# Kernel optimization log

Measured on AMD Instinct MI355X. Metric: run time of the kernel, lower is better.

## Reference

```python
import jax, jax.numpy as jnp
import numpy as np

B, S, EH2, DH, A = 128, 1024, 1024, 512, 512

def setup_inputs() -> dict:
    key = jax.random.key(0)
    k1, k2, k3, k4, k5 = jax.random.split(key, 5)
    scale_in = 1.0 / np.sqrt(EH2 + DH)
    scale_a = 1.0 / np.sqrt(A)
    return {
        "encoder_outputs": jax.random.normal(k1, (B, S, EH2), dtype=jnp.float32),
        "decoder_hidden": jax.random.normal(k2, (B, DH), dtype=jnp.float32),
        "src_mask": jnp.ones((B, S), dtype=jnp.int32),
        "W_attn": jax.random.normal(k3, (EH2 + DH, A), dtype=jnp.float32) * scale_in,
        "b_attn": jax.random.normal(k4, (A,), dtype=jnp.float32) * scale_in,
        "v": jax.random.normal(k5, (A,), dtype=jnp.float32) * scale_a,
    }

def reference(encoder_outputs, decoder_hidden, src_mask, W_attn, b_attn, v):
    # Split W_attn into encoder-part and decoder-part to avoid materializing
    # the [B,S,EH2+DH] concat (same math as Linear(cat(enc, dec_repeated))).
    W_enc = W_attn[:EH2]          # [EH2, A]
    W_dec = W_attn[EH2:]          # [DH, A]
    enc_proj = jnp.einsum('bse,ea->bsa', encoder_outputs, W_enc)  # [B,S,A]
    dec_proj = decoder_hidden @ W_dec                              # [B,A]
    energy = jnp.tanh(enc_proj + dec_proj[:, None, :] + b_attn)    # [B,S,A]
    scores = jnp.einsum('bsa,a->bs', energy, v)                    # [B,S]
    scores = jnp.where(src_mask == 0, jnp.float32(-1e10), scores)
    attn_weights = jax.nn.softmax(scores, axis=1)                  # [B,S]
    context = jnp.einsum('bs,bse->be', attn_weights, encoder_outputs)  # [B,EH2]
    return (context, attn_weights)
```

## Files before the change

kernel.cpp:

```cpp
#include <hip/hip_runtime.h>
#include <math.h>

#define BB   128
#define SS   1024
#define EH2  1024
#define DHD  512
#define AD   512
#define MTOT (BB*SS)
#define KDIM 1024

#define BM2   64
#define BK2   32
#define NSTEP (KDIM/BK2)

typedef __attribute__((ext_vector_type(8)))  short short8;
typedef __attribute__((ext_vector_type(16))) float f32x16;

static __device__ __forceinline__ unsigned short f2bf_rne(float x) {
    unsigned u = __float_as_uint(x);
    u += 0x7FFF + ((u >> 16) & 1);
    return (unsigned short)(u >> 16);
}

__global__ __launch_bounds__(256) void k0_wprep(
    const float* __restrict__ W, unsigned short* __restrict__ Wt)
{
    const int g     = blockIdx.x * 256 + threadIdx.x;
    const int lane  = g & 63;
    const int ct    = (g >> 6) & 15;
    const int kk2   = (g >> 10) & 1;
    const int ks    = g >> 11;
    const int col   = ct * 32 + (lane & 31);
    const int kbase = ks * 32 + kk2 * 16 + (lane >> 5) * 8;
    short8 out;
    #pragma unroll
    for (int j = 0; j < 8; ++j)
        out[j] = (short)f2bf_rne(W[(size_t)(kbase + j) * AD + col]);
    *(short8*)&Wt[(size_t)g * 8] = out;
}

__global__ __launch_bounds__(256) void k1_decproj(
    const float* __restrict__ dec,
    const float* __restrict__ Wdec,
    const float* __restrict__ bias,
    float* __restrict__ dec_proj)
{
    __shared__ float dls[DHD];
    const int b = blockIdx.x;
    const int t = threadIdx.x;
    for (int i = t; i < DHD; i += 256) dls[i] = dec[b * DHD + i];
    __syncthreads();
    float acc0 = bias[t];
    float acc1 = bias[t + 256];
    #pragma unroll 8
    for (int k = 0; k < DHD; ++k) {
        const float d = dls[k];
        acc0 += d * Wdec[(size_t)k * AD + t];
        acc1 += d * Wdec[(size_t)k * AD + t + 256];
    }
    dec_proj[b * AD + t]       = acc0;
    dec_proj[b * AD + t + 256] = acc1;
}

#define AS_IDX(hl, kk2, mt) (((hl) * 2 + (kk2)) * 2 + (mt))

__global__ __launch_bounds__(256, 2) void k2_gemm_score(
    const float* __restrict__ enc,
    const unsigned short* __restrict__ Wt,
    const float* __restrict__ dp,
    const float* __restrict__ v,
    float* __restrict__ scores)
{
    __shared__ unsigned short As[2][8][512];
    __shared__ float dp_l[AD], v_l[AD];
    __shared__ float sred[4][BM2];

    const int t     = threadIdx.x;
    const int wn    = t >> 6;
    const int lane  = t & 63;
    const int mbase = blockIdx.x * BM2;
    const int b     = blockIdx.x >> 4;

    dp_l[t]       = dp[b * AD + t];
    dp_l[t + 256] = dp[b * AD + t + 256];
    v_l[t]        = v[t];
    v_l[t + 256]  = v[t + 256];

    const int smt  = (t >> 6) & 1;
    const int skk2 = t >> 7;
    const int srow = smt * 32 + (lane & 31);
    const int skb  = skk2 * 16 + (lane >> 5) * 8;
    const float* aptr = enc + (size_t)(mbase + srow) * KDIM + skb;
    unsigned short* asH = &As[0][AS_IDX(0, skk2, smt)][lane * 8];
    unsigned short* asL = &As[0][AS_IDX(1, skk2, smt)][lane * 8];
    const int asStride = 8 * 512;

    const short8* bbase = (const short8*)Wt + wn * 256 + lane;

#define CONV_WRITE_A(buf_, xa_, xb_) do {                                   \
    const float xs_[8] = {xa_.x, xa_.y, xa_.z, xa_.w, xb_.x, xb_.y, xb_.z, xb_.w}; \
    short8 hi_, lo_;                                                        \
    _Pragma("unroll")                                                       \
    for (int j_ = 0; j_ < 8; ++j_) {                                        \
        const unsigned u_ = __float_as_uint(xs_[j_]);                       \
        hi_[j_] = (short)(u_ >> 16);                                        \
        lo_[j_] = (short)f2bf_rne(xs_[j_] - __uint_as_float(u_ & 0xFFFF0000u)); \
    }                                                                       \
    *(short8*)(asH + (buf_) * asStride) = hi_;                              \
    *(short8*)(asL + (buf_) * asStride) = lo_;                              \
} while (0)

    f32x16 acc[2][4];
    #pragma unroll
    for (int mi = 0; mi < 2; ++mi)
        #pragma unroll
        for (int n = 0; n < 4; ++n) acc[mi][n] = (f32x16)0.f;

    {
        const float4 xa = *(const float4*)(aptr);
        const float4 xb = *(const float4*)(aptr + 4);
        CONV_WRITE_A(0, xa, xb);
    }
    __syncthreads();

#define KSTEP(BUF, ks_)                                                      \
  {                                                                          \
    const bool pf = ((ks_) + 1 < NSTEP);                                     \
    float4 xa, xb;                                                           \
    if (pf) {                                                                \
        xa = *(const float4*)(aptr + ((ks_) + 1) * BK2);                     \
        xb = *(const float4*)(aptr + ((ks_) + 1) * BK2 + 4);                 \
    }                                                                        \
                                                                \
    {                                                                        \
        short8 bfr[4];                                                       \
        _Pragma("unroll")                                                    \
        for (int n = 0; n < 4; ++n) bfr[n] = bbase[(ks_) * 2048 + n * 64];   \
        const short8 aH0 = *(const short8*)&As[BUF][AS_IDX(0,0,0)][lane*8];  \
        const short8 aL0 = *(const short8*)&As[BUF][AS_IDX(1,0,0)][lane*8];  \
        const short8 aH1 = *(const short8*)&As[BUF][AS_IDX(0,0,1)][lane*8];  \
        const short8 aL1 = *(const short8*)&As[BUF][AS_IDX(1,0,1)][lane*8];  \
        __builtin_amdgcn_s_setprio(1);                                       \
        _Pragma("unroll")                                                    \
        for (int n = 0; n < 4; ++n) {                                        \
            acc[0][n] = __builtin_amdgcn_mfma_f32_32x32x16_bf16(aH0, bfr[n], acc[0][n], 0, 0, 0); \
            acc[0][n] = __builtin_amdgcn_mfma_f32_32x32x16_bf16(aL0, bfr[n], acc[0][n], 0, 0, 0); \
            acc[1][n] = __builtin_amdgcn_mfma_f32_32x32x16_bf16(aH1, bfr[n], acc[1][n], 0, 0, 0); \
            acc[1][n] = __builtin_amdgcn_mfma_f32_32x32x16_bf16(aL1, bfr[n], acc[1][n], 0, 0, 0); \
        }                                                                    \
        __builtin_amdgcn_s_setprio(0);                                       \
    }                                                                        \
                                                                \
    {                                                                        \
        short8 bfr[4];                                                       \
        _Pragma("unroll")                                                    \
        for (int n = 0; n < 4; ++n) bfr[n] = bbase[(ks_) * 2048 + 1024 + n * 64]; \
        const short8 aH0 = *(const short8*)&As[BUF][AS_IDX(0,1,0)][lane*8];  \
        const short8 aL0 = *(const short8*)&As[BUF][AS_IDX(1,1,0)][lane*8];  \
        const short8 aH1 = *(const short8*)&As[BUF][AS_IDX(0,1,1)][lane*8];  \
        const short8 aL1 = *(const short8*)&As[BUF][AS_IDX(1,1,1)][lane*8];  \
        __builtin_amdgcn_s_setprio(1);                                       \
        _Pragma("unroll")                                                    \
        for (int n = 0; n < 4; ++n) {                                        \
            acc[0][n] = __builtin_amdgcn_mfma_f32_32x32x16_bf16(aH0, bfr[n], acc[0][n], 0, 0, 0); \
            acc[0][n] = __builtin_amdgcn_mfma_f32_32x32x16_bf16(aL0, bfr[n], acc[0][n], 0, 0, 0); \
            acc[1][n] = __builtin_amdgcn_mfma_f32_32x32x16_bf16(aH1, bfr[n], acc[1][n], 0, 0, 0); \
            acc[1][n] = __builtin_amdgcn_mfma_f32_32x32x16_bf16(aL1, bfr[n], acc[1][n], 0, 0, 0); \
        }                                                                    \
        __builtin_amdgcn_s_setprio(0);                                       \
    }                                                                        \
    if (pf) CONV_WRITE_A((BUF) ^ 1, xa, xb);                                 \
    __syncthreads();                                                         \
  }

    for (int ks = 0; ks < NSTEP; ks += 2) {
        KSTEP(0, ks);
        KSTEP(1, ks + 1);
    }
#undef KSTEP
#undef CONV_WRITE_A

    const int c    = lane & 31;
    const int half = lane >> 5;
    float vv[4], dpv[4];
    #pragma unroll
    for (int n = 0; n < 4; ++n) {
        const int col = wn * 128 + n * 32 + c;
        vv[n]  = v_l[col];
        dpv[n] = dp_l[col];
    }
    #pragma unroll
    for (int mi = 0; mi < 2; ++mi) {
        float part[16];
        #pragma unroll
        for (int r = 0; r < 16; ++r) {
            float s = 0.f;
            #pragma unroll
            for (int n = 0; n < 4; ++n) {
                const float e  = acc[mi][n][r] + dpv[n];
                const float te = __expf(2.f * e);
                s += vv[n] * (1.f - __fdividef(2.f, te + 1.f));
            }
            part[r] = s;
        }
        #pragma unroll
        for (int off = 1; off < 32; off <<= 1)
            #pragma unroll
            for (int r = 0; r < 16; ++r)
                part[r] += __shfl_xor(part[r], off);
        if (c == 0) {
            #pragma unroll
            for (int r = 0; r < 16; ++r)
                sred[wn][mi * 32 + 4 * half + (r & 3) + 8 * (r >> 2)] = part[r];
        }
    }
    __syncthreads();
    if (t < BM2)
        scores[mbase + t] = sred[0][t] + sred[1][t] + sred[2][t] + sred[3][t];
}

__global__ __launch_bounds__(256) void k3_softmax(
    const float* __restrict__ sc,
    const int*   __restrict__ mask,
    float* __restrict__ wts)
{
    const int b = blockIdx.x;
    const int t = threadIdx.x;
    float local[4];
    float mx = -3.0e38f;
    #pragma unroll
    for (int r = 0; r < 4; ++r) {
        const int s = r * 256 + t;
        float val = sc[b * SS + s];
        if (mask[b * SS + s] == 0) val = -1.0e10f;
        local[r] = val;
        mx = fmaxf(mx, val);
    }
    #pragma unroll
    for (int off = 1; off < 64; off <<= 1) mx = fmaxf(mx, __shfl_xor(mx, off));
    __shared__ float redm[4], reds[4];
    if ((t & 63) == 0) redm[t >> 6] = mx;
    __syncthreads();
    mx = fmaxf(fmaxf(redm[0], redm[1]), fmaxf(redm[2], redm[3]));

    float sum = 0.f;
    #pragma unroll
    for (int r = 0; r < 4; ++r) { local[r] = __expf(local[r] - mx); sum += local[r]; }
    #pragma unroll
    for (int off = 1; off < 64; off <<= 1) sum += __shfl_xor(sum, off);
    if ((t & 63) == 0) reds[t >> 6] = sum;
    __syncthreads();
    sum = reds[0] + reds[1] + reds[2] + reds[3];
    const float inv = 1.f / sum;
    #pragma unroll
    for (int r = 0; r < 4; ++r) wts[b * SS + r * 256 + t] = local[r] * inv;
}

#define SCHUNK 128
__global__ __launch_bounds__(256) void k4_context(
    const float* __restrict__ enc,
    const float* __restrict__ wts,
    float* __restrict__ ctx)
{
    const int b  = blockIdx.x;
    const int ch = blockIdx.y;
    const int e4 = threadIdx.x * 4;
    const float* encb = enc + (size_t)b * SS * EH2 + (size_t)ch * SCHUNK * EH2;
    const float* wb   = wts + b * SS + ch * SCHUNK;
    float4 acc = make_float4(0.f, 0.f, 0.f, 0.f);
    #pragma unroll 4
    for (int s = 0; s < SCHUNK; ++s) {
        const float w = wb[s];
        const float4 ev = *(const float4*)&encb[(size_t)s * EH2 + e4];
        acc.x = fmaf(w, ev.x, acc.x);
        acc.y = fmaf(w, ev.y, acc.y);
        acc.z = fmaf(w, ev.z, acc.z);
        acc.w = fmaf(w, ev.w, acc.w);
    }
    atomicAdd(&ctx[b * EH2 + e4 + 0], acc.x);
    atomicAdd(&ctx[b * EH2 + e4 + 1], acc.y);
    atomicAdd(&ctx[b * EH2 + e4 + 2], acc.z);
    atomicAdd(&ctx[b * EH2 + e4 + 3], acc.w);
}

extern "C" void kernel_launch(void* const* d_in, const int* in_sizes, int n_in,
                              void* d_out, int out_size, void* d_ws, size_t ws_size,
                              hipStream_t stream) {
    const float* enc    = (const float*)d_in[0];
    const float* dec    = (const float*)d_in[1];
    const int*   mask   = (const int*)  d_in[2];
    const float* W      = (const float*)d_in[3];
    const float* b_attn = (const float*)d_in[4];
    const float* v      = (const float*)d_in[5];

    float* out = (float*)d_out;
    float* ctx = out;
    float* wts = out + BB * EH2;

    unsigned short* Wt  = (unsigned short*)d_ws;
    float* dec_proj     = (float*)((char*)d_ws + (1 << 20));
    float* scores       = dec_proj + BB * AD;

    hipMemsetAsync(ctx, 0, (size_t)BB * EH2 * sizeof(float), stream);

    k0_wprep<<<256, 256, 0, stream>>>(W, Wt);

    k1_decproj<<<BB, 256, 0, stream>>>(dec, W + (size_t)EH2 * AD, b_attn, dec_proj);

    k2_gemm_score<<<MTOT / BM2, 256, 0, stream>>>(enc, Wt, dec_proj, v, scores);

    k3_softmax<<<BB, 256, 0, stream>>>(scores, mask, wts);

    dim3 g4(BB, SS / SCHUNK);
    k4_context<<<g4, 256, 0, stream>>>(enc, wts, ctx);
}
```

Before: 1.028 ms.

## Software-pipeline B fragment loads in GEMM and replace atomic context reduction

In the fused GEMM+score kernel, B-operand register fragments are now double-buffered: the next half-step's weights are loaded into registers before the current MFMA block issues, so global load latency overlaps with matrix math. The context stage swaps the memset plus float atomics for a partial-sum kernel that writes per-chunk results to workspace, followed by a small reduction kernel. The atomic path is kept as a fallback when the workspace is too small. This adds register pressure, one extra kernel launch and extra workspace traffic.

```diff
diff --git a/kernel.cpp b/kernel.cpp
--- a/kernel.cpp
+++ b/kernel.cpp
@@ -95,7 +95,15 @@
     unsigned short* asL = &As[0][AS_IDX(1, skk2, smt)][lane * 8];
     const int asStride = 8 * 512;
 
-    const short8* bbase = (const short8*)Wt + wn * 256 + lane;
+    const short8* bb8 = (const short8*)Wt + wn * 256 + lane;
+
+    short8 bA[4], bB[4];
+
+#define LOADB_H(ks_, kk2_, R) do {                                          \
+    _Pragma("unroll")                                                       \
+    for (int n_ = 0; n_ < 4; ++n_)                                          \
+        R[n_] = bb8[(ks_) * 2048 + (kk2_) * 1024 + n_ * 64];                \
+} while (0)
 
 #define CONV_WRITE_A(buf_, xa_, xb_) do {                                   \
     const float xs_[8] = {xa_.x, xa_.y, xa_.z, xa_.w, xb_.x, xb_.y, xb_.z, xb_.w}; \
@@ -110,6 +118,22 @@
     *(short8*)(asL + (buf_) * asStride) = lo_;                              \
 } while (0)
 
+#define MFMA_H(BUF, KK2, R) do {                                            \
+    const short8 aH0 = *(const short8*)&As[BUF][AS_IDX(0,KK2,0)][lane*8];   \
+    const short8 aL0 = *(const short8*)&As[BUF][AS_IDX(1,KK2,0)][lane*8];   \
+    const short8 aH1 = *(const short8*)&As[BUF][AS_IDX(0,KK2,1)][lane*8];   \
+    const short8 aL1 = *(const short8*)&As[BUF][AS_IDX(1,KK2,1)][lane*8];   \
+    __builtin_amdgcn_s_setprio(1);                                          \
+    _Pragma("unroll")                                                       \
+    for (int n_ = 0; n_ < 4; ++n_) {                                        \
+        acc[0][n_] = __builtin_amdgcn_mfma_f32_32x32x16_bf16(aH0, R[n_], acc[0][n_], 0, 0, 0); \
+        acc[0][n_] = __builtin_amdgcn_mfma_f32_32x32x16_bf16(aL0, R[n_], acc[0][n_], 0, 0, 0); \
+        acc[1][n_] = __builtin_amdgcn_mfma_f32_32x32x16_bf16(aH1, R[n_], acc[1][n_], 0, 0, 0); \
+        acc[1][n_] = __builtin_amdgcn_mfma_f32_32x32x16_bf16(aL1, R[n_], acc[1][n_], 0, 0, 0); \
+    }                                                                       \
+    __builtin_amdgcn_s_setprio(0);                                          \
+} while (0)
+
     f32x16 acc[2][4];
     #pragma unroll
     for (int mi = 0; mi < 2; ++mi)
@@ -119,6 +143,7 @@
     {
         const float4 xa = *(const float4*)(aptr);
         const float4 xb = *(const float4*)(aptr + 4);
+        LOADB_H(0, 0, bA);
         CONV_WRITE_A(0, xa, xb);
     }
     __syncthreads();
@@ -126,49 +151,15 @@
 #define KSTEP(BUF, ks_)                                                      \
   {                                                                          \
     const bool pf = ((ks_) + 1 < NSTEP);                                     \
+    LOADB_H((ks_), 1, bB);                         \
     float4 xa, xb;                                                           \
     if (pf) {                                                                \
         xa = *(const float4*)(aptr + ((ks_) + 1) * BK2);                     \
         xb = *(const float4*)(aptr + ((ks_) + 1) * BK2 + 4);                 \
     }                                                                        \
-                                                                \
-    {                                                                        \
-        short8 bfr[4];                                                       \
-        _Pragma("unroll")                                                    \
-        for (int n = 0; n < 4; ++n) bfr[n] = bbase[(ks_) * 2048 + n * 64];   \
-        const short8 aH0 = *(const short8*)&As[BUF][AS_IDX(0,0,0)][lane*8];  \
-        const short8 aL0 = *(const short8*)&As[BUF][AS_IDX(1,0,0)][lane*8];  \
-        const short8 aH1 = *(const short8*)&As[BUF][AS_IDX(0,0,1)][lane*8];  \
-        const short8 aL1 = *(const short8*)&As[BUF][AS_IDX(1,0,1)][lane*8];  \
-        __builtin_amdgcn_s_setprio(1);                                       \
-        _Pragma("unroll")                                                    \
-        for (int n = 0; n < 4; ++n) {                                        \
-            acc[0][n] = __builtin_amdgcn_mfma_f32_32x32x16_bf16(aH0, bfr[n], acc[0][n], 0, 0, 0); \
-            acc[0][n] = __builtin_amdgcn_mfma_f32_32x32x16_bf16(aL0, bfr[n], acc[0][n], 0, 0, 0); \
-            acc[1][n] = __builtin_amdgcn_mfma_f32_32x32x16_bf16(aH1, bfr[n], acc[1][n], 0, 0, 0); \
-            acc[1][n] = __builtin_amdgcn_mfma_f32_32x32x16_bf16(aL1, bfr[n], acc[1][n], 0, 0, 0); \
-        }                                                                    \
-        __builtin_amdgcn_s_setprio(0);                                       \
-    }                                                                        \
-                                                                \
-    {                                                                        \
-        short8 bfr[4];                                                       \
-        _Pragma("unroll")                                                    \
-        for (int n = 0; n < 4; ++n) bfr[n] = bbase[(ks_) * 2048 + 1024 + n * 64]; \
-        const short8 aH0 = *(const short8*)&As[BUF][AS_IDX(0,1,0)][lane*8];  \
-        const short8 aL0 = *(const short8*)&As[BUF][AS_IDX(1,1,0)][lane*8];  \
-        const short8 aH1 = *(const short8*)&As[BUF][AS_IDX(0,1,1)][lane*8];  \
-        const short8 aL1 = *(const short8*)&As[BUF][AS_IDX(1,1,1)][lane*8];  \
-        __builtin_amdgcn_s_setprio(1);                                       \
-        _Pragma("unroll")                                                    \
-        for (int n = 0; n < 4; ++n) {                                        \
-            acc[0][n] = __builtin_amdgcn_mfma_f32_32x32x16_bf16(aH0, bfr[n], acc[0][n], 0, 0, 0); \
-            acc[0][n] = __builtin_amdgcn_mfma_f32_32x32x16_bf16(aL0, bfr[n], acc[0][n], 0, 0, 0); \
-            acc[1][n] = __builtin_amdgcn_mfma_f32_32x32x16_bf16(aH1, bfr[n], acc[1][n], 0, 0, 0); \
-            acc[1][n] = __builtin_amdgcn_mfma_f32_32x32x16_bf16(aL1, bfr[n], acc[1][n], 0, 0, 0); \
-        }                                                                    \
-        __builtin_amdgcn_s_setprio(0);                                       \
-    }                                                                        \
+    MFMA_H(BUF, 0, bA);                      \
+    if (pf) LOADB_H((ks_) + 1, 0, bA);                \
+    MFMA_H(BUF, 1, bB);                               \
     if (pf) CONV_WRITE_A((BUF) ^ 1, xa, xb);                                 \
     __syncthreads();                                                         \
   }
@@ -178,7 +169,9 @@
         KSTEP(1, ks + 1);
     }
 #undef KSTEP
+#undef LOADB_H
 #undef CONV_WRITE_A
+#undef MFMA_H
 
     const int c    = lane & 31;
     const int half = lane >> 5;
@@ -256,20 +249,57 @@
     for (int r = 0; r < 4; ++r) wts[b * SS + r * 256 + t] = local[r] * inv;
 }
 
-#define SCHUNK 128
-__global__ __launch_bounds__(256) void k4_context(
+#define SCHUNK4 128
+__global__ __launch_bounds__(256) void k4a_partial(
     const float* __restrict__ enc,
     const float* __restrict__ wts,
-    float* __restrict__ ctx)
+    float* __restrict__ part)
 {
     const int b  = blockIdx.x;
     const int ch = blockIdx.y;
     const int e4 = threadIdx.x * 4;
-    const float* encb = enc + (size_t)b * SS * EH2 + (size_t)ch * SCHUNK * EH2;
-    const float* wb   = wts + b * SS + ch * SCHUNK;
+    const float* encb = enc + (size_t)b * SS * EH2 + (size_t)ch * SCHUNK4 * EH2;
+    const float* wb   = wts + b * SS + ch * SCHUNK4;
     float4 acc = make_float4(0.f, 0.f, 0.f, 0.f);
     #pragma unroll 4
-    for (int s = 0; s < SCHUNK; ++s) {
+    for (int s = 0; s < SCHUNK4; ++s) {
+        const float w = wb[s];
+        const float4 ev = *(const float4*)&encb[(size_t)s * EH2 + e4];
+        acc.x = fmaf(w, ev.x, acc.x);
+        acc.y = fmaf(w, ev.y, acc.y);
+        acc.z = fmaf(w, ev.z, acc.z);
+        acc.w = fmaf(w, ev.w, acc.w);
+    }
+    *(float4*)&part[((size_t)b * 8 + ch) * EH2 + e4] = acc;
+}
+
+__global__ __launch_bounds__(256) void k4b_reduce(
+    const float* __restrict__ part,
+    float* __restrict__ ctx)
+{
+    const int b  = blockIdx.x;
+    const int e4 = threadIdx.x * 4;
+    float4 acc = make_float4(0.f, 0.f, 0.f, 0.f);
+    #pragma unroll
+    for (int ch = 0; ch < 8; ++ch) {
+        const float4 p = *(const float4*)&part[((size_t)b * 8 + ch) * EH2 + e4];
+        acc.x += p.x; acc.y += p.y; acc.z += p.z; acc.w += p.w;
+    }
+    *(float4*)&ctx[b * EH2 + e4] = acc;
+}
+
+__global__ __launch_bounds__(256) void k4_context_atomic(
+    const float* __restrict__ enc, const float* __restrict__ wts,
+    float* __restrict__ ctx)
+{
+    const int b  = blockIdx.x;
+    const int ch = blockIdx.y;
+    const int e4 = threadIdx.x * 4;
+    const float* encb = enc + (size_t)b * SS * EH2 + (size_t)ch * SCHUNK4 * EH2;
+    const float* wb   = wts + b * SS + ch * SCHUNK4;
+    float4 acc = make_float4(0.f, 0.f, 0.f, 0.f);
+    #pragma unroll 4
+    for (int s = 0; s < SCHUNK4; ++s) {
         const float w = wb[s];
         const float4 ev = *(const float4*)&encb[(size_t)s * EH2 + e4];
         acc.x = fmaf(w, ev.x, acc.x);
@@ -300,8 +330,8 @@
     unsigned short* Wt  = (unsigned short*)d_ws;
     float* dec_proj     = (float*)((char*)d_ws + (1 << 20));
     float* scores       = dec_proj + BB * AD;
-
-    hipMemsetAsync(ctx, 0, (size_t)BB * EH2 * sizeof(float), stream);
+    float* part         = scores + MTOT;
+    const size_t ws_needed = (1u << 20) + (size_t)(BB * AD + MTOT + BB * 8 * EH2) * 4;
 
     k0_wprep<<<256, 256, 0, stream>>>(W, Wt);
 
@@ -311,6 +341,12 @@
 
     k3_softmax<<<BB, 256, 0, stream>>>(scores, mask, wts);
 
-    dim3 g4(BB, SS / SCHUNK);
-    k4_context<<<g4, 256, 0, stream>>>(enc, wts, ctx);
-}
+    dim3 g4(BB, SS / SCHUNK4);
+    if (ws_size >= ws_needed) {
+        k4a_partial<<<g4, 256, 0, stream>>>(enc, wts, part);
+        k4b_reduce<<<BB, 256, 0, stream>>>(part, ctx);
+    } else {
+        hipMemsetAsync(ctx, 0, (size_t)BB * EH2 * sizeof(float), stream);
+        k4_context_atomic<<<g4, 256, 0, stream>>>(enc, wts, ctx);
+    }
+}
```

Measured after the change: 975.1 us. 1.05x faster.
